# Kernel tuning notes

Measured on AMD Instinct MI355X. Metric: run time of the kernel, lower is better.

Reference implementation:

```python
import jax, jax.numpy as jnp
import numpy as np

# Module hyperparameters (from init_kwargs)
B, C, T, H, W = 2, 128, 4, 64, 64
NHEADS = 32
SH, SW = 4, 4          # scales: patch size in H and W
GROUPS = C // 4        # GroupNorm groups = dim // 4
EPS = 1e-5


def _rel_index(t_, h_, w_):
    """(N,N) int32 index into the (2T-1)*(2h-1)*(2w-1) relative-position table."""
    tt = np.arange(t_); yy = np.arange(h_); xx = np.arange(w_)
    coords = np.stack(np.meshgrid(tt, yy, xx, indexing='ij'), -1).reshape(-1, 3)  # (N,3)
    rel = coords[:, None, :] - coords[None, :, :]                                 # (N,N,3)
    rel = rel + np.array([t_ - 1, h_ - 1, w_ - 1])
    idx = (rel[..., 0] * (2 * h_ - 1) + rel[..., 1]) * (2 * w_ - 1) + rel[..., 2]
    return idx.astype(np.int32)


def setup_inputs() -> dict:
    key = jax.random.key(0)
    ks = jax.random.split(key, 6)
    h, w = H // SH, W // SW
    table_sz = (2 * T - 1) * (2 * h - 1) * (2 * w - 1)
    inp = {
        "x": jax.random.normal(ks[0], (B, C, T, H, W), jnp.float32),
        "Wq": jax.random.normal(ks[1], (C, C), jnp.float32) / np.sqrt(C).astype(np.float32),
        "Wk": jax.random.normal(ks[2], (C, C), jnp.float32) / np.sqrt(C).astype(np.float32),
        "Wv": jax.random.normal(ks[3], (C, C), jnp.float32) / np.sqrt(C).astype(np.float32),
        "gq_gamma": jnp.ones((C,), jnp.float32), "gq_beta": jnp.zeros((C,), jnp.float32),
        "gk_gamma": jnp.ones((C,), jnp.float32), "gk_beta": jnp.zeros((C,), jnp.float32),
        "gv_gamma": jnp.ones((C,), jnp.float32), "gv_beta": jnp.zeros((C,), jnp.float32),
        "rel_table": jax.random.normal(ks[4], (NHEADS, table_sz), jnp.float32) * 0.02,
        "rel_index": jnp.asarray(_rel_index(T, h, w)),
    }
    return inp


def _group_norm(z, gamma, beta, groups, eps=EPS):
    b, c = z.shape[:2]
    zg = z.reshape(b, groups, c // groups, *z.shape[2:])
    mu = zg.mean(axis=(2, 3, 4, 5), keepdims=True)
    var = jnp.mean(jnp.square(zg - mu), axis=(2, 3, 4, 5), keepdims=True)
    zg = (zg - mu) * jax.lax.rsqrt(var + eps)
    zn = zg.reshape(z.shape)
    return zn * gamma[None, :, None, None, None] + beta[None, :, None, None, None]


def reference(x, Wq, Wk, Wv, gq_gamma, gq_beta, gk_gamma, gk_beta,
              gv_gamma, gv_beta, rel_table, rel_index):
    b, c, t, hh, ww = x.shape
    h, w = hh // SH, ww // SW
    n = t * h * w           # patch tokens
    p = SH * SW             # pixels per patch
    d = c // NHEADS         # head dim

    # 1x1x1 projections (pointwise conv == channel matmul) + GroupNorm
    q = _group_norm(jnp.einsum('bcthw,oc->bothw', x, Wq), gq_gamma, gq_beta, GROUPS)
    k = _group_norm(jnp.einsum('bcthw,oc->bothw', x, Wk), gk_gamma, gk_beta, GROUPS)
    v = _group_norm(jnp.einsum('bcthw,oc->bothw', x, Wv), gv_gamma, gv_beta, GROUPS)

    def to_patches(z):  # (b,c,t,H,W) -> (b,heads,d,N,P)
        z = z.reshape(b, NHEADS, d, t, h, SH, w, SW)
        z = z.transpose(0, 1, 2, 3, 4, 6, 5, 7)
        return z.reshape(b, NHEADS, d, n, p)

    qp = to_patches(q).mean(-1)     # pooled patch queries (b,g,d,N)
    kp = to_patches(k).mean(-1)     # pooled patch keys    (b,g,d,N)
    vp = to_patches(v)              # full-res values      (b,g,d,N,P)

    scale = 1.0 / jnp.sqrt(jnp.float32(d))
    logits = jnp.einsum('bgdn,bgdm->bgnm', qp, kp) * scale
    logits = logits + rel_table[:, rel_index][None]   # relative position bias (1,g,N,N)
    attn = jax.nn.softmax(logits, axis=-1)

    out = jnp.einsum('bgnm,bgdmp->bgdnp', attn, vp)   # (b,g,d,N,P)
    out = out.reshape(b, NHEADS, d, t, h, w, SH, SW).transpose(0, 1, 2, 3, 4, 6, 5, 7)
    out = out.reshape(b, c, t, hh, ww)                # (B,C,T,H,W) after outer permute
    return out
```

## Files before the change

### kernel.cpp

```cpp
#include <hip/hip_runtime.h>
#include <hip/hip_bf16.h>

#define B_ 2
#define C_ 128
#define G_ 32
#define N_ 1024
#define S_ 16384
#define TABLE_ 6727
#define EPS_ 1e-5f
#define LOG2E_ 1.44269504f
#define PSTB_ 64
#define NSTRIP_ 128

typedef __hip_bfloat16 bf16;
typedef __attribute__((ext_vector_type(8))) short short8;
typedef __attribute__((ext_vector_type(4))) float f32x4;

#if __has_builtin(__builtin_amdgcn_exp2f)
#define EXP2(x) __builtin_amdgcn_exp2f(x)
#else
#define EXP2(x) __expf((x) * 0.69314718056f)
#endif

__device__ __forceinline__ float bf2f(bf16 v) { return __bfloat162float(v); }
__device__ __forceinline__ float bits2f(unsigned u) { return __uint_as_float(u); }
__device__ __forceinline__ int dflag(const void* gq) {
  return (((const unsigned*)gq)[0] != 0x3F803F80u) ? 1 : 0;
}
__device__ __forceinline__ float ldcv(const void* p, int i, int fl) {
  return fl ? ((const float*)p)[i] : bf2f(((const bf16*)p)[i]);
}
__device__ __forceinline__ size_t spidx(int ttm, int b, int g) {
  return ((size_t)(((ttm * B_ + b) * G_) + g)) << 7;
}

__global__ __launch_bounds__(256) void proj_kernel(
    const void* __restrict__ x, const void* __restrict__ Wq,
    const void* __restrict__ Wk, const void* __restrict__ Wv,
    const void* __restrict__ gq,
    float* __restrict__ qpart, float* __restrict__ kpart,
    bf16* __restrict__ vpt, float* __restrict__ sp)
{
  __shared__ bf16 xs[128 * 128];
  __shared__ bf16 vs[8192];
  const int tid = threadIdx.x, lane = tid & 63, w = tid >> 6;
  const int s0 = blockIdx.x * 128;
  const int oh = blockIdx.y;
  const int b  = blockIdx.z;
  const int fl = dflag(gq);

  {
    const int cb = tid >> 4, sb = tid & 15;
    const size_t gc0 = (size_t)b * C_ * S_ + (size_t)(cb * 8) * S_ + s0 + sb * 8;
    union U8 { short8 v; ushort h[8]; };
    U8 in[8];
    if (fl) {
#pragma unroll
      for (int j = 0; j < 8; ++j) {
        const float* xp = (const float*)x + gc0 + (size_t)j * S_;
        const float4 a = *(const float4*)xp, b2 = *(const float4*)(xp + 4);
        union { short8 s; bf16 hh[8]; } u;
        u.hh[0] = (bf16)a.x;  u.hh[1] = (bf16)a.y;  u.hh[2] = (bf16)a.z;  u.hh[3] = (bf16)a.w;
        u.hh[4] = (bf16)b2.x; u.hh[5] = (bf16)b2.y; u.hh[6] = (bf16)b2.z; u.hh[7] = (bf16)b2.w;
        in[j].v = u.s;
      }
    } else {
#pragma unroll
      for (int j = 0; j < 8; ++j)
        in[j].v = *(const short8*)((const bf16*)x + gc0 + (size_t)j * S_);
    }
#pragma unroll
    for (int si = 0; si < 8; ++si) {
      U8 o;
#pragma unroll
      for (int i = 0; i < 8; ++i) o.h[i] = in[i].h[si];
      const int s = sb * 8 + si;
      *(short8*)&xs[s * 128 + ((cb ^ si ^ (sb & 7)) << 3)] = o.v;
    }
  }

  const int ow = oh * 4 + w;
  const int quad = lane >> 4;
  const int om = ow * 16 + (lane & 15);
  const void* const Ws[3] = {Wq, Wk, Wv};
  short8 afr[3][4];
#pragma unroll
  for (int tt = 0; tt < 3; ++tt)
#pragma unroll
    for (int kk = 0; kk < 4; ++kk) {
      const int off = om * 128 + kk * 32 + quad * 8;
      if (fl) {
        const float* wp = (const float*)Ws[tt] + off;
        const float4 a = *(const float4*)wp, bb = *(const float4*)(wp + 4);
        union { short8 s; bf16 h[8]; } u;
        u.h[0] = (bf16)a.x;  u.h[1] = (bf16)a.y;  u.h[2] = (bf16)a.z;  u.h[3] = (bf16)a.w;
        u.h[4] = (bf16)bb.x; u.h[5] = (bf16)bb.y; u.h[6] = (bf16)bb.z; u.h[7] = (bf16)bb.w;
        afr[tt][kk] = u.s;
      } else {
        afr[tt][kk] = *(const short8*)((const bf16*)Ws[tt] + off);
      }
    }
  __syncthreads();

  float ssum[3] = {0.f, 0.f, 0.f}, ssq[3] = {0.f, 0.f, 0.f};
  float psq[4][4] = {}, psk[4][4] = {};
  const int sl = lane & 15;
#pragma unroll
  for (int st = 0; st < 8; ++st) {
    f32x4 acc[3] = {{0,0,0,0},{0,0,0,0},{0,0,0,0}};
    const int srow = st * 16 + sl;
    const int rxor = (sl & 7) ^ ((st << 1) & 7) ^ (sl >> 3);
#pragma unroll
    for (int kk = 0; kk < 4; ++kk) {
      const short8 bv = *(const short8*)
          &xs[srow * 128 + ((((kk << 2) | quad) ^ rxor) << 3)];
      acc[0] = __builtin_amdgcn_mfma_f32_16x16x32_bf16(afr[0][kk], bv, acc[0], 0, 0, 0);
      acc[1] = __builtin_amdgcn_mfma_f32_16x16x32_bf16(afr[1][kk], bv, acc[1], 0, 0, 0);
      acc[2] = __builtin_amdgcn_mfma_f32_16x16x32_bf16(afr[2][kk], bv, acc[2], 0, 0, 0);
    }
    const int pIdx = (st >> 2) * 4 + (sl & 3);
    const int xp = (st & 3) * 4 + (sl >> 2);
#pragma unroll
    for (int r = 0; r < 4; ++r) {
      const float vq = acc[0][r], vk = acc[1][r], vv = acc[2][r];
      ssum[0] += vq; ssq[0] += vq * vq;
      ssum[1] += vk; ssq[1] += vk * vk;
      ssum[2] += vv; ssq[2] += vv * vv;
      float aq = vq + __shfl_xor(vq, 1); aq += __shfl_xor(aq, 2);
      float ak = vk + __shfl_xor(vk, 1); ak += __shfl_xor(ak, 2);
      psq[r][st & 3] += aq;
      psk[r][st & 3] += ak;
      const int o_loc = w * 16 + quad * 4 + r;
      vs[(o_loc * 8 + pIdx) * 16 + xp] = (bf16)vv;
    }
  }

  {
    const int c = sl & 3, wxl = sl >> 2;
    const int t = s0 >> 12;
    const int yy0 = (s0 >> 6) & 63;
    const int hy = yy0 >> 2, rp = (yy0 >> 1) & 1;
    const int nbase = t * 256 + hy * 16;
    const size_t pb = ((size_t)(b * 2 + rp) * N_ + nbase) * C_ + ow * 16 + quad * 4 + c;
#pragma unroll
    for (int j = 0; j < 4; ++j) {
      float vq = psq[0][j];
      if (c == 1) vq = psq[1][j];
      if (c == 2) vq = psq[2][j];
      if (c == 3) vq = psq[3][j];
      float vk = psk[0][j];
      if (c == 1) vk = psk[1][j];
      if (c == 2) vk = psk[2][j];
      if (c == 3) vk = psk[3][j];
      qpart[pb + (size_t)(j * 4 + wxl) * C_] = vq;
      kpart[pb + (size_t)(j * 4 + wxl) * C_] = vk;
    }
  }

#pragma unroll
  for (int tt = 0; tt < 3; ++tt) {
#pragma unroll
    for (int off = 1; off < 16; off <<= 1) {
      ssum[tt] += __shfl_xor(ssum[tt], off);
      ssq[tt]  += __shfl_xor(ssq[tt], off);
    }
    if ((lane & 15) == 0) {
      const int grp = ow * 4 + quad;
      sp[spidx(tt * 2 + 0, b, grp) + blockIdx.x] = ssum[tt];
      sp[spidx(tt * 2 + 1, b, grp) + blockIdx.x] = ssq[tt];
    }
  }
  __syncthreads();

  const int rowp0 = (s0 >> 6) & 63;
  const int mIdx0 = (s0 >> 12) * 256 + (rowp0 >> 2) * 16;
  for (int cid = tid; cid < 1024; cid += 256) {
    const int half = cid & 1, run = cid >> 1;
    const int o_loc = run >> 3, pIdx = run & 7;
    const int o = oh * 64 + o_loc;
    const int gg = o >> 2, dd = o & 3;
    const int colv = dd * 16 + (rowp0 & 3) * 4 + pIdx;
    bf16* dst = vpt + ((size_t)(b * G_ + gg) * 64 + colv) * N_ + mIdx0 + half * 8;
    *(short8*)dst = *(const short8*)&vs[run * 16 + half * 8];
  }
}

__global__ __launch_bounds__(256, 4) void attn_kernel(
    const float* __restrict__ qpart, const float* __restrict__ kpart,
    const bf16* __restrict__ vpt, const void* __restrict__ rt,
    const void* __restrict__ gq, const void* __restrict__ bq,
    const void* __restrict__ gk, const void* __restrict__ bk,
    const void* __restrict__ gv, const void* __restrict__ bv,
    const float* __restrict__ sp, void* __restrict__ outv)
{
  const int g = blockIdx.y, b = blockIdx.z;
  const int tid = threadIdx.x, lane = tid & 63, w = tid >> 6;
  const int nw = blockIdx.x * 64;
  const int fl = dflag(gq);
  __shared__ __align__(16) char smem[37816];
  bf16* Vlds = (bf16*)smem;
  bf16* bldm = (bf16*)(smem + 8192);
  bf16* pldw = (bf16*)(smem + 13216) + w * 16 * PSTB_;
  bf16* klds = (bf16*)(smem + 21408);
  float* red = (float*)(smem + 37792);

  const int col = lane & 15, quad = lane >> 4;
  const size_t bg = (size_t)(b * G_ + g);
  const short* vpb = (const short*)vpt + bg * 64 * N_;
  const int vn0 = tid >> 3, kb8 = tid & 7;

  short8 st[2];
#pragma unroll
  for (int i = 0; i < 2; ++i)
    st[i] = *(const short8*)(vpb + (size_t)(i * 32 + vn0) * N_ + 0 * 64 + kb8 * 8);

  if (w < 2) {
#pragma unroll
    for (int j = 0; j < 3; ++j) {
      const float* a = sp + spidx(w + 2 * j, b, g);
      float v = a[lane] + a[lane + 64];
      v += __shfl_xor(v, 1);  v += __shfl_xor(v, 2);  v += __shfl_xor(v, 4);
      v += __shfl_xor(v, 8);  v += __shfl_xor(v, 16); v += __shfl_xor(v, 32);
      if (lane == 0) red[w + 2 * j] = v;
    }
  }

  const int tn = nw >> 8, yb = (nw >> 4) & 15;
  for (int i = tid; i < 2508; i += 256) {
    const int row = i / 33, d = i - row * 33;
    if (d < 31) {
      const int tm = row / 19, dyi = row - tm * 19;
      const int dt = tn - tm + 3;
      const int dy = yb + dyi;
      bldm[row * 33 + d] = (bf16)(ldcv(rt, g * TABLE_ + (dt * 31 + dy) * 31 + d, fl) * LOG2E_);
    }
  }
  __syncthreads();

  const float muq = red[0] * (1.f / 65536.f);
  const float rq = rsqrtf(red[1] * (1.f / 65536.f) - muq * muq + EPS_);
  const float muk = red[2] * (1.f / 65536.f);
  const float rk = rsqrtf(red[3] * (1.f / 65536.f) - muk * muk + EPS_);

  short8 af = {0, 0, 0, 0, 0, 0, 0, 0};
  if (quad < 2) {
    const int n = nw + w * 16 + col;
    const f32x4 q0 = *(const f32x4*)&qpart[((size_t)(b * 2 + 0) * N_ + n) * C_ + g * 4];
    const f32x4 q1 = *(const f32x4*)&qpart[((size_t)(b * 2 + 1) * N_ + n) * C_ + g * 4];
    union { short8 s; bf16 h[8]; } u;
#pragma unroll
    for (int d = 0; d < 4; ++d) {
      const int c = g * 4 + d;
      const float sq = q0[d] + q1[d];
      const float qn = (sq * 0.0625f - muq) * rq * ldcv(gq, c, fl) + ldcv(bq, c, fl);
      const float qs = qn * (0.5f * LOG2E_);
      const bf16 qh = (bf16)qs;
      u.h[d] = qh; u.h[4 + d] = (bf16)(qs - bf2f(qh));
    }
    af = u.s;
  }

  {
    float gkv[4], bkv[4];
#pragma unroll
    for (int d = 0; d < 4; ++d) {
      gkv[d] = ldcv(gk, g * 4 + d, fl);
      bkv[d] = ldcv(bk, g * 4 + d, fl);
    }
#pragma unroll
    for (int i = 0; i < 4; ++i) {
      const int n = i * 256 + tid;
      const f32x4 k0 = *(const f32x4*)&kpart[((size_t)(b * 2 + 0) * N_ + n) * C_ + g * 4];
      const f32x4 k1 = *(const f32x4*)&kpart[((size_t)(b * 2 + 1) * N_ + n) * C_ + g * 4];
      union { short8 s; bf16 h[8]; } u;
#pragma unroll
      for (int d = 0; d < 4; ++d) {
        const float kn = ((k0[d] + k1[d]) * 0.0625f - muk) * rk * gkv[d] + bkv[d];
        const bf16 kh = (bf16)kn;
        u.h[d] = kh; u.h[4 + d] = (bf16)(kn - bf2f(kh));
      }
      *(short8*)&klds[n * 8] = u.s;
    }
  }
  __syncthreads();

  const short* klds_s = (const short*)klds;
  const short onebits = (short)0x3F80;
  const short8 ones8 = {onebits, onebits, onebits, onebits,
                        onebits, onebits, onebits, onebits};
  f32x4 acco[4] = {{0,0,0,0},{0,0,0,0},{0,0,0,0},{0,0,0,0}};
  f32x4 accs = {0.f, 0.f, 0.f, 0.f};

  ushort4 kv[4], kvn[4];
#pragma unroll
  for (int t = 0; t < 4; ++t)
    kv[t] = *(const ushort4*)(klds_s + ((0 * 4 + t) * 16 + col) * 8 + (quad & 1) * 4);

  for (int ch = 0; ch < 16; ++ch) {
    if (ch > 0) __syncthreads();
#pragma unroll
    for (int i = 0; i < 2; ++i) {
      const int n = i * 32 + vn0;
      *(short8*)&Vlds[n * 64 + ((kb8 ^ (n & 7)) << 3)] = st[i];
    }
    __syncthreads();
    if (ch < 15) {
#pragma unroll
      for (int i = 0; i < 2; ++i)
        st[i] = *(const short8*)(vpb + (size_t)(i * 32 + vn0) * N_ + (ch + 1) * 64 + kb8 * 8);
#pragma unroll
      for (int t = 0; t < 4; ++t)
        kvn[t] = *(const ushort4*)(klds_s + (((ch + 1) * 4 + t) * 16 + col) * 8 + (quad & 1) * 4);
    }
#pragma unroll
    for (int mt4 = 0; mt4 < 4; ++mt4) {
      const int mt = ch * 4 + mt4;
      const int tm = mt >> 4, ym = mt & 15;
      const short8 bf8 = {(short)kv[mt4].x, (short)kv[mt4].y, (short)kv[mt4].z, (short)kv[mt4].w,
                          (short)kv[mt4].x, (short)kv[mt4].y, (short)kv[mt4].z, (short)kv[mt4].w};
      f32x4 acc = {0.f, 0.f, 0.f, 0.f};
      acc = __builtin_amdgcn_mfma_f32_16x16x32_bf16(af, bf8, acc, 0, 0, 0);
      const int bbase = (tm * 19 + (w + 15 - ym)) * 33 + 15 + quad * 4 - col;
#pragma unroll
      for (int r = 0; r < 4; ++r) {
        const float e = EXP2(acc[r] + bf2f(bldm[bbase + r]));
        const int row = quad * 4 + r;
        pldw[row * PSTB_ + (((mt4 * 2 + (col >> 3)) ^ (row & 7)) << 3) + (col & 7)] = (bf16)e;
      }
    }
    __builtin_amdgcn_s_setprio(1);
#pragma unroll
    for (int ks = 0; ks < 2; ++ks) {
      const short8 a2 = *(const short8*)&pldw[col * PSTB_ + (((ks * 4 + quad) ^ (col & 7)) << 3)];
      accs = __builtin_amdgcn_mfma_f32_16x16x32_bf16(a2, ones8, accs, 0, 0, 0);
#pragma unroll
      for (int cc = 0; cc < 4; ++cc) {
        const int n = cc * 16 + col;
        const int kb = ks * 4 + quad;
        const short8 b2 = *(const short8*)&Vlds[n * 64 + ((kb ^ (n & 7)) << 3)];
        acco[cc] = __builtin_amdgcn_mfma_f32_16x16x32_bf16(a2, b2, acco[cc], 0, 0, 0);
      }
    }
    __builtin_amdgcn_s_setprio(0);
    if (ch < 15) {
#pragma unroll
      for (int t = 0; t < 4; ++t) kv[t] = kvn[t];
    }
  }

  __syncthreads();
  const float mu = red[4] * (1.f / 65536.f);
  const float rs = rsqrtf(red[5] * (1.f / 65536.f) - mu * mu + EPS_);
  const int sh = col >> 2, sw = col & 3;
  const size_t obase = (size_t)(b * C_ + g * 4) * S_ + tn * 4096 + (yb + w) * 256;
  if (!fl) {
    bf16* ost = (bf16*)(smem + w * 2048);
#pragma unroll
    for (int cc = 0; cc < 4; ++cc) {
      const int c = g * 4 + cc;
      const float alpha = rs * ldcv(gv, c, fl);
      const float beta = ldcv(bv, c, fl) - mu * alpha;
#pragma unroll
      for (int r = 0; r < 4; ++r) {
        const int xp = quad * 4 + r;
        ost[cc * 256 + sh * 64 + xp * 4 + sw] = (bf16)(alpha * (acco[cc][r] / accs[r]) + beta);
      }
    }
#pragma unroll
    for (int i = 0; i < 2; ++i) {
      const int e = (i * 64 + lane) * 8;
      const int cc = e >> 8, rem = e & 255;
      *(short8*)((bf16*)outv + obase + (size_t)cc * S_ + rem) = *(const short8*)&ost[e];
    }
  } else {
    float* ostf = (float*)smem + w * 1024;
#pragma unroll
    for (int cc = 0; cc < 4; ++cc) {
      const int c = g * 4 + cc;
      const float alpha = rs * ldcv(gv, c, fl);
      const float beta = ldcv(bv, c, fl) - mu * alpha;
#pragma unroll
      for (int r = 0; r < 4; ++r) {
        const int xp = quad * 4 + r;
        ostf[cc * 256 + sh * 64 + xp * 4 + sw] = alpha * (acco[cc][r] / accs[r]) + beta;
      }
    }
#pragma unroll
    for (int i = 0; i < 4; ++i) {
      const int e = (i * 64 + lane) * 4;
      const int cc = e >> 8, rem = e & 255;
      *(float4*)((float*)outv + obase + (size_t)cc * S_ + rem) = *(const float4*)&ostf[e];
    }
  }
}

extern "C" void kernel_launch(void* const* d_in, const int* in_sizes, int n_in,
                              void* d_out, int out_size, void* d_ws, size_t ws_size,
                              hipStream_t stream) {
  (void)in_sizes; (void)n_in; (void)out_size; (void)ws_size;
  const void* x  = d_in[0];
  const void* Wq = d_in[1];
  const void* Wk = d_in[2];
  const void* Wv = d_in[3];
  const void* gq = d_in[4];
  const void* bq = d_in[5];
  const void* gk = d_in[6];
  const void* bk = d_in[7];
  const void* gv = d_in[8];
  const void* bv = d_in[9];
  const void* rel_table = d_in[10];

  bf16*  vpt  = (bf16*)d_ws;
  float* qpart = (float*)(vpt + (size_t)B_ * G_ * 64 * N_);
  float* kpart = qpart + (size_t)B_ * 2 * N_ * C_;
  float* sp    = kpart + (size_t)B_ * 2 * N_ * C_;

  proj_kernel<<<dim3(NSTRIP_, 2, B_), 256, 0, stream>>>(
      x, Wq, Wk, Wv, gq, qpart, kpart, vpt, sp);
  attn_kernel<<<dim3(16, G_, B_), 256, 0, stream>>>(
      qpart, kpart, vpt, rel_table, gq, bq, gk, bk, gv, bv, sp, d_out);
}
```

Before: 162.2 us.

## Keep softmax probabilities in registers and double-buffer V tiles in LDS

The attention loop now computes logits transposed (K as the A operand, Q as B), so each lane's exp2 outputs can feed a 16x16x16 bf16 MFMA directly as the A fragment. This removes the per-wave LDS round trip for P and the extra ones-vector MFMA that built row sums; row sums are now accumulated in registers and reduced with shuffles. V tiles are double-buffered in LDS, which cuts one barrier per chunk. The q/k partial-sum layout also moves to channel-major, making the proj stores and attn loads scalar-strided, which may coalesce differently. The risks are more register pressure and the smaller K=16 MFMAs.

New measurement: 174.9 us. +7.8%, slower.

```diff
diff --git a/kernel.cpp b/kernel.cpp
--- a/kernel.cpp
+++ b/kernel.cpp
@@ -9,17 +9,27 @@
 #define TABLE_ 6727
 #define EPS_ 1e-5f
 #define LOG2E_ 1.44269504f
-#define PSTB_ 64
 #define NSTRIP_ 128
 
 typedef __hip_bfloat16 bf16;
 typedef __attribute__((ext_vector_type(8))) short short8;
+typedef __attribute__((ext_vector_type(4))) short short4v;
 typedef __attribute__((ext_vector_type(4))) float f32x4;
 
 #if __has_builtin(__builtin_amdgcn_exp2f)
 #define EXP2(x) __builtin_amdgcn_exp2f(x)
 #else
 #define EXP2(x) __expf((x) * 0.69314718056f)
+#endif
+
+#if __has_builtin(__builtin_amdgcn_mfma_f32_16x16x16bf16_1k)
+#define MFMA16(a, b, c) __builtin_amdgcn_mfma_f32_16x16x16bf16_1k(a, b, c, 0, 0, 0)
+#else
+static __device__ __forceinline__ f32x4 mfma16_asm(short4v a, short4v b, f32x4 c) {
+  asm volatile("v_mfma_f32_16x16x16_bf16 %0, %1, %2, %0" : "+v"(c) : "v"(a), "v"(b));
+  return c;
+}
+#define MFMA16(a, b, c) mfma16_asm(a, b, c)
 #endif
 
 __device__ __forceinline__ float bf2f(bf16 v) { return __bfloat162float(v); }
@@ -141,7 +151,7 @@
     const int yy0 = (s0 >> 6) & 63;
     const int hy = yy0 >> 2, rp = (yy0 >> 1) & 1;
     const int nbase = t * 256 + hy * 16;
-    const size_t pb = ((size_t)(b * 2 + rp) * N_ + nbase) * C_ + ow * 16 + quad * 4 + c;
+    const size_t pb = ((size_t)((b * 2 + rp) * C_ + ow * 16 + quad * 4 + c)) * N_ + nbase;
 #pragma unroll
     for (int j = 0; j < 4; ++j) {
       float vq = psq[0][j];
@@ -152,8 +162,8 @@
       if (c == 1) vk = psk[1][j];
       if (c == 2) vk = psk[2][j];
       if (c == 3) vk = psk[3][j];
-      qpart[pb + (size_t)(j * 4 + wxl) * C_] = vq;
-      kpart[pb + (size_t)(j * 4 + wxl) * C_] = vk;
+      qpart[pb + j * 4 + wxl] = vq;
+      kpart[pb + j * 4 + wxl] = vk;
     }
   }
 
@@ -198,9 +208,9 @@
   const int nw = blockIdx.x * 64;
   const int fl = dflag(gq);
   __shared__ __align__(16) char smem[37816];
-  bf16* Vlds = (bf16*)smem;
-  bf16* bldm = (bf16*)(smem + 8192);
-  bf16* pldw = (bf16*)(smem + 13216) + w * 16 * PSTB_;
+  bf16* V0   = (bf16*)smem;
+  bf16* V1   = (bf16*)(smem + 8192);
+  bf16* bldm = (bf16*)(smem + 16384);
   bf16* klds = (bf16*)(smem + 21408);
   float* red = (float*)(smem + 37792);
 
@@ -242,22 +252,23 @@
   const float muk = red[2] * (1.f / 65536.f);
   const float rk = rsqrtf(red[3] * (1.f / 65536.f) - muk * muk + EPS_);
 
-  short8 af = {0, 0, 0, 0, 0, 0, 0, 0};
+  short8 bq8 = {0, 0, 0, 0, 0, 0, 0, 0};
   if (quad < 2) {
     const int n = nw + w * 16 + col;
-    const f32x4 q0 = *(const f32x4*)&qpart[((size_t)(b * 2 + 0) * N_ + n) * C_ + g * 4];
-    const f32x4 q1 = *(const f32x4*)&qpart[((size_t)(b * 2 + 1) * N_ + n) * C_ + g * 4];
     union { short8 s; bf16 h[8]; } u;
 #pragma unroll
     for (int d = 0; d < 4; ++d) {
       const int c = g * 4 + d;
-      const float sq = q0[d] + q1[d];
+      const float sq = qpart[((size_t)((b * 2 + 0) * C_ + c)) * N_ + n]
+                     + qpart[((size_t)((b * 2 + 1) * C_ + c)) * N_ + n];
       const float qn = (sq * 0.0625f - muq) * rq * ldcv(gq, c, fl) + ldcv(bq, c, fl);
       const float qs = qn * (0.5f * LOG2E_);
       const bf16 qh = (bf16)qs;
       u.h[d] = qh; u.h[4 + d] = (bf16)(qs - bf2f(qh));
     }
-    af = u.s;
+    const int hb = (quad & 1) * 4;
+#pragma unroll
+    for (int j = 0; j < 4; ++j) { bq8[j] = u.s[hb + j]; bq8[4 + j] = u.s[hb + j]; }
   }
 
   {
@@ -270,12 +281,13 @@
 #pragma unroll
     for (int i = 0; i < 4; ++i) {
       const int n = i * 256 + tid;
-      const f32x4 k0 = *(const f32x4*)&kpart[((size_t)(b * 2 + 0) * N_ + n) * C_ + g * 4];
-      const f32x4 k1 = *(const f32x4*)&kpart[((size_t)(b * 2 + 1) * N_ + n) * C_ + g * 4];
       union { short8 s; bf16 h[8]; } u;
 #pragma unroll
       for (int d = 0; d < 4; ++d) {
-        const float kn = ((k0[d] + k1[d]) * 0.0625f - muk) * rk * gkv[d] + bkv[d];
+        const int c = g * 4 + d;
+        const float sk = kpart[((size_t)((b * 2 + 0) * C_ + c)) * N_ + n]
+                       + kpart[((size_t)((b * 2 + 1) * C_ + c)) * N_ + n];
+        const float kn = (sk * 0.0625f - muk) * rk * gkv[d] + bkv[d];
         const bf16 kh = (bf16)kn;
         u.h[d] = kh; u.h[4 + d] = (bf16)(kn - bf2f(kh));
       }
@@ -284,69 +296,77 @@
   }
   __syncthreads();
 
-  const short* klds_s = (const short*)klds;
-  const short onebits = (short)0x3F80;
-  const short8 ones8 = {onebits, onebits, onebits, onebits,
-                        onebits, onebits, onebits, onebits};
+  short8 kf[4], kfn[4];
+#pragma unroll
+  for (int mt = 0; mt < 4; ++mt)
+    kf[mt] = *(const short8*)&klds[(size_t)(0 * 64 + mt * 16 + col) * 8];
+
+#pragma unroll
+  for (int i = 0; i < 2; ++i) {
+    const int n = i * 32 + vn0;
+    *(short8*)&V0[n * 64 + ((kb8 ^ (n & 7)) << 3)] = st[i];
+  }
+  __syncthreads();
+
   f32x4 acco[4] = {{0,0,0,0},{0,0,0,0},{0,0,0,0},{0,0,0,0}};
-  f32x4 accs = {0.f, 0.f, 0.f, 0.f};
-
-  ushort4 kv[4], kvn[4];
-#pragma unroll
-  for (int t = 0; t < 4; ++t)
-    kv[t] = *(const ushort4*)(klds_s + ((0 * 4 + t) * 16 + col) * 8 + (quad & 1) * 4);
+  float srow = 0.f;
 
   for (int ch = 0; ch < 16; ++ch) {
-    if (ch > 0) __syncthreads();
-#pragma unroll
-    for (int i = 0; i < 2; ++i) {
-      const int n = i * 32 + vn0;
-      *(short8*)&Vlds[n * 64 + ((kb8 ^ (n & 7)) << 3)] = st[i];
-    }
-    __syncthreads();
+    const bf16* Vb = (ch & 1) ? V1 : V0;
     if (ch < 15) {
 #pragma unroll
       for (int i = 0; i < 2; ++i)
         st[i] = *(const short8*)(vpb + (size_t)(i * 32 + vn0) * N_ + (ch + 1) * 64 + kb8 * 8);
 #pragma unroll
-      for (int t = 0; t < 4; ++t)
-        kvn[t] = *(const ushort4*)(klds_s + (((ch + 1) * 4 + t) * 16 + col) * 8 + (quad & 1) * 4);
-    }
+      for (int mt = 0; mt < 4; ++mt)
+        kfn[mt] = *(const short8*)&klds[(size_t)((ch + 1) * 64 + mt * 16 + col) * 8];
+    }
+    __builtin_amdgcn_s_setprio(1);
 #pragma unroll
     for (int mt4 = 0; mt4 < 4; ++mt4) {
       const int mt = ch * 4 + mt4;
       const int tm = mt >> 4, ym = mt & 15;
-      const short8 bf8 = {(short)kv[mt4].x, (short)kv[mt4].y, (short)kv[mt4].z, (short)kv[mt4].w,
-                          (short)kv[mt4].x, (short)kv[mt4].y, (short)kv[mt4].z, (short)kv[mt4].w};
+      const int bb = (tm * 19 + (w + 15 - ym)) * 33 + 15 + col - quad * 4;
+      float bs[4];
+#pragma unroll
+      for (int r = 0; r < 4; ++r) bs[r] = bf2f(bldm[bb - r]);
       f32x4 acc = {0.f, 0.f, 0.f, 0.f};
-      acc = __builtin_amdgcn_mfma_f32_16x16x32_bf16(af, bf8, acc, 0, 0, 0);
-      const int bbase = (tm * 19 + (w + 15 - ym)) * 33 + 15 + quad * 4 - col;
+      acc = __builtin_amdgcn_mfma_f32_16x16x32_bf16(kf[mt4], bq8, acc, 0, 0, 0);
+      union { short4v s4; bf16 h[4]; } pa;
 #pragma unroll
       for (int r = 0; r < 4; ++r) {
-        const float e = EXP2(acc[r] + bf2f(bldm[bbase + r]));
-        const int row = quad * 4 + r;
-        pldw[row * PSTB_ + (((mt4 * 2 + (col >> 3)) ^ (row & 7)) << 3) + (col & 7)] = (bf16)e;
-      }
-    }
-    __builtin_amdgcn_s_setprio(1);
-#pragma unroll
-    for (int ks = 0; ks < 2; ++ks) {
-      const short8 a2 = *(const short8*)&pldw[col * PSTB_ + (((ks * 4 + quad) ^ (col & 7)) << 3)];
-      accs = __builtin_amdgcn_mfma_f32_16x16x32_bf16(a2, ones8, accs, 0, 0, 0);
+        const float e = EXP2(acc[r] + bs[r]);
+        srow += e;
+        pa.h[r] = (bf16)e;
+      }
+      const int kbb = mt4 * 2 + (quad >> 1);
 #pragma unroll
       for (int cc = 0; cc < 4; ++cc) {
         const int n = cc * 16 + col;
-        const int kb = ks * 4 + quad;
-        const short8 b2 = *(const short8*)&Vlds[n * 64 + ((kb ^ (n & 7)) << 3)];
-        acco[cc] = __builtin_amdgcn_mfma_f32_16x16x32_bf16(a2, b2, acco[cc], 0, 0, 0);
+        union { ushort4 u; short4v s4; } vb;
+        vb.u = *(const ushort4*)&Vb[n * 64 + ((kbb ^ (n & 7)) << 3) + (quad & 1) * 4];
+        acco[cc] = MFMA16(pa.s4, vb.s4, acco[cc]);
       }
     }
     __builtin_amdgcn_s_setprio(0);
     if (ch < 15) {
 #pragma unroll
-      for (int t = 0; t < 4; ++t) kv[t] = kvn[t];
-    }
-  }
+      for (int mt = 0; mt < 4; ++mt) kf[mt] = kfn[mt];
+      bf16* Vn = ((ch + 1) & 1) ? V1 : V0;
+#pragma unroll
+      for (int i = 0; i < 2; ++i) {
+        const int n = i * 32 + vn0;
+        *(short8*)&Vn[n * 64 + ((kb8 ^ (n & 7)) << 3)] = st[i];
+      }
+      __syncthreads();
+    }
+  }
+
+  srow += __shfl_xor(srow, 16);
+  srow += __shfl_xor(srow, 32);
+  f32x4 fs;
+#pragma unroll
+  for (int r = 0; r < 4; ++r) fs[r] = __shfl(srow, quad * 4 + r);
 
   __syncthreads();
   const float mu = red[4] * (1.f / 65536.f);
@@ -363,7 +383,7 @@
 #pragma unroll
       for (int r = 0; r < 4; ++r) {
         const int xp = quad * 4 + r;
-        ost[cc * 256 + sh * 64 + xp * 4 + sw] = (bf16)(alpha * (acco[cc][r] / accs[r]) + beta);
+        ost[cc * 256 + sh * 64 + xp * 4 + sw] = (bf16)(alpha * (acco[cc][r] / fs[r]) + beta);
       }
     }
 #pragma unroll
@@ -382,7 +402,7 @@
 #pragma unroll
       for (int r = 0; r < 4; ++r) {
         const int xp = quad * 4 + r;
-        ostf[cc * 256 + sh * 64 + xp * 4 + sw] = alpha * (acco[cc][r] / accs[r]) + beta;
+        ostf[cc * 256 + sh * 64 + xp * 4 + sw] = alpha * (acco[cc][r] / fs[r]) + beta;
       }
     }
 #pragma unroll
@@ -412,8 +432,8 @@
 
   bf16*  vpt  = (bf16*)d_ws;
   float* qpart = (float*)(vpt + (size_t)B_ * G_ * 64 * N_);
-  float* kpart = qpart + (size_t)B_ * 2 * N_ * C_;
-  float* sp    = kpart + (size_t)B_ * 2 * N_ * C_;
+  float* kpart = qpart + (size_t)B_ * 2 * C_ * N_;
+  float* sp    = kpart + (size_t)B_ * 2 * C_ * N_;
 
   proj_kernel<<<dim3(NSTRIP_, 2, B_), 256, 0, stream>>>(
       x, Wq, Wk, Wv, gq, qpart, kpart, vpt, sp);
```

## Transpose pooled q/k partials to channel-major and compute softmax row sums via shuffles

Applied to the files above, without the earlier changes.

Changes the qpart/kpart workspace layout from n-major to channel-major so that proj_kernel's partial stores become contiguous along n. attn_kernel's loads change from one f32x4 per position to four scalar loads per position, which are coalesced across threads. It also drops the ones-vector MFMA that computed softmax denominators. Instead it accumulates exp values in fp32 registers and reduces them with cross-lane shuffles after the loop, removing an MFMA from the inner loop at the cost of extra adds and a final reduction.

New measurement: 156.1 us. 1.04x faster.

```diff
diff --git a/kernel.cpp b/kernel.cpp
--- a/kernel.cpp
+++ b/kernel.cpp
@@ -141,7 +141,7 @@
     const int yy0 = (s0 >> 6) & 63;
     const int hy = yy0 >> 2, rp = (yy0 >> 1) & 1;
     const int nbase = t * 256 + hy * 16;
-    const size_t pb = ((size_t)(b * 2 + rp) * N_ + nbase) * C_ + ow * 16 + quad * 4 + c;
+    const size_t pb = ((size_t)((b * 2 + rp) * C_ + ow * 16 + quad * 4 + c)) * N_ + nbase;
 #pragma unroll
     for (int j = 0; j < 4; ++j) {
       float vq = psq[0][j];
@@ -152,8 +152,8 @@
       if (c == 1) vk = psk[1][j];
       if (c == 2) vk = psk[2][j];
       if (c == 3) vk = psk[3][j];
-      qpart[pb + (size_t)(j * 4 + wxl) * C_] = vq;
-      kpart[pb + (size_t)(j * 4 + wxl) * C_] = vk;
+      qpart[pb + j * 4 + wxl] = vq;
+      kpart[pb + j * 4 + wxl] = vk;
     }
   }
 
@@ -245,13 +245,12 @@
   short8 af = {0, 0, 0, 0, 0, 0, 0, 0};
   if (quad < 2) {
     const int n = nw + w * 16 + col;
-    const f32x4 q0 = *(const f32x4*)&qpart[((size_t)(b * 2 + 0) * N_ + n) * C_ + g * 4];
-    const f32x4 q1 = *(const f32x4*)&qpart[((size_t)(b * 2 + 1) * N_ + n) * C_ + g * 4];
     union { short8 s; bf16 h[8]; } u;
 #pragma unroll
     for (int d = 0; d < 4; ++d) {
       const int c = g * 4 + d;
-      const float sq = q0[d] + q1[d];
+      const float sq = qpart[((size_t)((b * 2 + 0) * C_ + c)) * N_ + n]
+                     + qpart[((size_t)((b * 2 + 1) * C_ + c)) * N_ + n];
       const float qn = (sq * 0.0625f - muq) * rq * ldcv(gq, c, fl) + ldcv(bq, c, fl);
       const float qs = qn * (0.5f * LOG2E_);
       const bf16 qh = (bf16)qs;
@@ -270,12 +269,13 @@
 #pragma unroll
     for (int i = 0; i < 4; ++i) {
       const int n = i * 256 + tid;
-      const f32x4 k0 = *(const f32x4*)&kpart[((size_t)(b * 2 + 0) * N_ + n) * C_ + g * 4];
-      const f32x4 k1 = *(const f32x4*)&kpart[((size_t)(b * 2 + 1) * N_ + n) * C_ + g * 4];
       union { short8 s; bf16 h[8]; } u;
 #pragma unroll
       for (int d = 0; d < 4; ++d) {
-        const float kn = ((k0[d] + k1[d]) * 0.0625f - muk) * rk * gkv[d] + bkv[d];
+        const int c = g * 4 + d;
+        const float sk = kpart[((size_t)((b * 2 + 0) * C_ + c)) * N_ + n]
+                       + kpart[((size_t)((b * 2 + 1) * C_ + c)) * N_ + n];
+        const float kn = (sk * 0.0625f - muk) * rk * gkv[d] + bkv[d];
         const bf16 kh = (bf16)kn;
         u.h[d] = kh; u.h[4 + d] = (bf16)(kn - bf2f(kh));
       }
@@ -285,11 +285,8 @@
   __syncthreads();
 
   const short* klds_s = (const short*)klds;
-  const short onebits = (short)0x3F80;
-  const short8 ones8 = {onebits, onebits, onebits, onebits,
-                        onebits, onebits, onebits, onebits};
   f32x4 acco[4] = {{0,0,0,0},{0,0,0,0},{0,0,0,0},{0,0,0,0}};
-  f32x4 accs = {0.f, 0.f, 0.f, 0.f};
+  float rs4[4] = {0.f, 0.f, 0.f, 0.f};
 
   ushort4 kv[4], kvn[4];
 #pragma unroll
@@ -324,6 +321,7 @@
 #pragma unroll
       for (int r = 0; r < 4; ++r) {
         const float e = EXP2(acc[r] + bf2f(bldm[bbase + r]));
+        rs4[r] += e;
         const int row = quad * 4 + r;
         pldw[row * PSTB_ + (((mt4 * 2 + (col >> 3)) ^ (row & 7)) << 3) + (col & 7)] = (bf16)e;
       }
@@ -332,7 +330,6 @@
 #pragma unroll
     for (int ks = 0; ks < 2; ++ks) {
       const short8 a2 = *(const short8*)&pldw[col * PSTB_ + (((ks * 4 + quad) ^ (col & 7)) << 3)];
-      accs = __builtin_amdgcn_mfma_f32_16x16x32_bf16(a2, ones8, accs, 0, 0, 0);
 #pragma unroll
       for (int cc = 0; cc < 4; ++cc) {
         const int n = cc * 16 + col;
@@ -346,6 +343,14 @@
 #pragma unroll
       for (int t = 0; t < 4; ++t) kv[t] = kvn[t];
     }
+  }
+
+#pragma unroll
+  for (int r = 0; r < 4; ++r) {
+    rs4[r] += __shfl_xor(rs4[r], 1);
+    rs4[r] += __shfl_xor(rs4[r], 2);
+    rs4[r] += __shfl_xor(rs4[r], 4);
+    rs4[r] += __shfl_xor(rs4[r], 8);
   }
 
   __syncthreads();
@@ -363,7 +368,7 @@
 #pragma unroll
       for (int r = 0; r < 4; ++r) {
         const int xp = quad * 4 + r;
-        ost[cc * 256 + sh * 64 + xp * 4 + sw] = (bf16)(alpha * (acco[cc][r] / accs[r]) + beta);
+        ost[cc * 256 + sh * 64 + xp * 4 + sw] = (bf16)(alpha * (acco[cc][r] / rs4[r]) + beta);
       }
     }
 #pragma unroll
@@ -382,7 +387,7 @@
 #pragma unroll
       for (int r = 0; r < 4; ++r) {
         const int xp = quad * 4 + r;
-        ostf[cc * 256 + sh * 64 + xp * 4 + sw] = alpha * (acco[cc][r] / accs[r]) + beta;
+        ostf[cc * 256 + sh * 64 + xp * 4 + sw] = alpha * (acco[cc][r] / rs4[r]) + beta;
       }
     }
 #pragma unroll
@@ -412,8 +417,8 @@
 
   bf16*  vpt  = (bf16*)d_ws;
   float* qpart = (float*)(vpt + (size_t)B_ * G_ * 64 * N_);
-  float* kpart = qpart + (size_t)B_ * 2 * N_ * C_;
-  float* sp    = kpart + (size_t)B_ * 2 * N_ * C_;
+  float* kpart = qpart + (size_t)B_ * 2 * C_ * N_;
+  float* sp    = kpart + (size_t)B_ * 2 * C_ * N_;
 
   proj_kernel<<<dim3(NSTRIP_, 2, B_), 256, 0, stream>>>(
       x, Wq, Wk, Wv, gq, qpart, kpart, vpt, sp);
```
